# Performance work log

Measured on AMD Instinct MI355X. Metric: run time of the kernel, lower is better.

## Reference

```python
import jax, jax.numpy as jnp
import numpy as np
from jax import lax

N = 256        # graph nodes (== conv5 channels)
C = 128        # diff-pool clusters
E = 4096       # number of edges
EPS = 1e-15    # PyG dense_diff_pool entropy eps


def setup_inputs():
    key = jax.random.key(0)
    ks = jax.random.split(key, 24)
    def rn(k, shape, scale):
        return jax.random.normal(k, shape, dtype=jnp.float32) * scale
    inp = {
        "inputs": jax.random.normal(ks[0], (1, 3, 512, 512), dtype=jnp.float32),
        "edge_index": jax.random.randint(ks[1], (2, E), 0, N, dtype=jnp.int32),
    }
    convs = [(3, 32), (32, 64), (64, 128), (128, 256), (256, 256)]
    for i, (ci, co) in enumerate(convs):
        inp[f"w{i+1}"] = rn(ks[2 + i], (co, ci, 3, 3), 0.05)
        inp[f"b{i+1}"] = jnp.zeros((co,), jnp.float32)
    sages = [(256, 2), (256, 128), (2, 2)]
    for i, (ci, co) in enumerate(sages):
        inp[f"s{i+1}_wl"] = rn(ks[10 + 3 * i], (ci, co), 0.1)
        inp[f"s{i+1}_wr"] = rn(ks[11 + 3 * i], (ci, co), 0.1)
        inp[f"s{i+1}_b"] = jnp.zeros((co,), jnp.float32)
    return inp


def _conv_block(x, w, b):
    # 3x3 SAME conv -> relu -> 2x2 max pool (stride 2), NCHW layout
    x = lax.conv_general_dilated(x, w, (1, 1), 'SAME',
                                 dimension_numbers=('NCHW', 'OIHW', 'NCHW'))
    x = jax.nn.relu(x + b[None, :, None, None])
    return lax.reduce_window(x, -jnp.inf, lax.max,
                             (1, 1, 2, 2), (1, 1, 2, 2), 'VALID')


def _sage(x, src, dst, wl, wr, b, n):
    # PyG SAGEConv(normalize=False): lin_l(mean_{src->dst} x_src) + lin_r(x)
    tot = jax.ops.segment_sum(x[src], dst, num_segments=n)
    cnt = jax.ops.segment_sum(jnp.ones((dst.shape[0],), x.dtype), dst, num_segments=n)
    agg = jnp.where(cnt[:, None] > 0, tot / jnp.maximum(cnt, 1.0)[:, None], 0.0)
    return agg @ wl + b + x @ wr


def reference(inputs, edge_index, w1, b1, w2, b2, w3, b3, w4, b4, w5, b5,
              s1_wl, s1_wr, s1_b, s2_wl, s2_wr, s2_b, s3_wl, s3_wr, s3_b):
    x = inputs
    for w, b in ((w1, b1), (w2, b2), (w3, b3), (w4, b4), (w5, b5)):
        x = _conv_block(x, w, b)
    org = x.reshape(N, N)  # (256 channels, 16*16 spatial) -> node features
    src, dst = edge_index[0], edge_index[1]
    x1 = _sage(org, src, dst, s1_wl, s1_wr, s1_b, N)  # (256, 2)
    s = _sage(org, src, dst, s2_wl, s2_wr, s2_b, N)   # (256, 128)
    # dense adjacency (duplicate edges accumulate, matching scipy coo.todense())
    adj = jnp.zeros((N, N), org.dtype).at[src, dst].add(1.0)
    # dense_diff_pool
    s_soft = jax.nn.softmax(s, axis=-1)
    x_pool = s_soft.T @ x1               # (128, 2)
    adj_pool = s_soft.T @ adj @ s_soft   # (128, 128)
    link_loss = jnp.linalg.norm(adj - s_soft @ s_soft.T) / (N * N)
    ent_loss = (-s_soft * jnp.log(s_soft + EPS)).sum(-1).mean()
    nodes = jnp.tanh(x_pool)             # (128, 2)
    # per-row argmax-equality thresholding (vectorized: rows are independent)
    row_max = adj_pool.max(axis=1, keepdims=True)
    edge_bin = (adj_pool == row_max).astype(org.dtype)  # (128, 128)
    # sage3 over the binarized dense adjacency (equivalent to dense_to_sparse + SAGEConv)
    indeg = edge_bin.sum(axis=0)
    agg = jnp.where(indeg[:, None] > 0,
                    (edge_bin.T @ nodes) / jnp.maximum(indeg, 1.0)[:, None], 0.0)
    out = agg @ s3_wl + s3_b + nodes @ s3_wr  # (128, 2)
    return out.reshape(-1), link_loss, ent_loss, nodes, edge_bin
```

## Files before the change

kernel.cpp:

```cpp
#include <hip/hip_runtime.h>
#include <math.h>

#define NN 256
#define NE 4096
#define NC 128

using short8  = __attribute__((ext_vector_type(8))) short;
using short4v = __attribute__((ext_vector_type(4))) short;
using f32x4   = __attribute__((ext_vector_type(4))) float;

static __device__ __forceinline__ unsigned short f2bf(float x) {
    unsigned u = __float_as_uint(x);
    unsigned r = (u + 0x7FFF + ((u >> 16) & 1)) >> 16;
    return (unsigned short)r;
}

static __device__ __forceinline__ float block_sum_256(float v, float* red4) {
    #pragma unroll
    for (int o = 32; o > 0; o >>= 1) v += __shfl_xor(v, o);
    __syncthreads();
    if ((threadIdx.x & 63) == 0) red4[threadIdx.x >> 6] = v;
    __syncthreads();
    return (red4[0] + red4[1]) + (red4[2] + red4[3]);
}

__global__ void wfrag_zero_all(const float* __restrict__ w1, const float* __restrict__ w2,
                               const float* __restrict__ w3, const float* __restrict__ w4,
                               const float* __restrict__ w5,
                               unsigned short* __restrict__ f1, unsigned short* __restrict__ f2,
                               unsigned short* __restrict__ f3, unsigned short* __restrict__ f4,
                               unsigned short* __restrict__ f5, float* __restrict__ adjz)
{
    int b = blockIdx.x;
    if (b >= 478) {
        adjz[(b - 478) * 256 + threadIdx.x] = 0.f;
        return;
    }
    if (b == 477) {
        int idx = threadIdx.x;
        int lane = idx & 63, rest = idx >> 6;
        int g = rest & 1, slot = rest >> 1;
        int oc = g * 16 + (lane & 15);
        short8 v;
        #pragma unroll
        for (int j = 0; j < 8; ++j) {
            int k = (lane >> 4) * 8 + j;
            float wv = 0.f;
            if (slot == 0) {
                int tap = k >> 2, ch = k & 3;
                if (ch < 3) wv = w1[oc * 27 + ch * 9 + tap];
            } else {
                if (k < 3) wv = w1[oc * 27 + k * 9 + 8];
            }
            v[j] = (short)f2bf(wv);
        }
        *(short8*)&f1[(size_t)idx * 8] = v;
        return;
    }
    const float* w; unsigned short* f; int CIN, NG, NCH, base;
    if (b < 9)        { w = w2; f = f2; CIN = 32;  NG = 4;  NCH = 1; base = 0;   }
    else if (b < 45)  { w = w3; f = f3; CIN = 64;  NG = 8;  NCH = 2; base = 9;   }
    else if (b < 189) { w = w4; f = f4; CIN = 128; NG = 16; NCH = 4; base = 45;  }
    else              { w = w5; f = f5; CIN = 256; NG = 16; NCH = 8; base = 189; }
    int idx = (b - base) * 256 + threadIdx.x;
    int lane = idx & 63, rest = idx >> 6;
    int c = rest % NCH; rest /= NCH;
    int g = rest % NG;  int t = rest / NG;
    if (t >= 9) return;
    int oc = g * 16 + (lane & 15);
    int cin0 = c * 32 + (lane >> 4) * 8;
    short8 v;
    #pragma unroll
    for (int j = 0; j < 8; ++j) {
        v[j] = (short)f2bf(w[((size_t)oc * CIN + cin0 + j) * 9 + t]);
    }
    *(short8*)&f[(size_t)idx * 8] = v;
}

__global__ __launch_bounds__(256) void conv1_adj_kernel(
    const float* __restrict__ in, const unsigned short* __restrict__ wf1,
    const float* __restrict__ bias, unsigned short* __restrict__ out,
    const int* __restrict__ src, const int* __restrict__ dst,
    float* __restrict__ adj, float* __restrict__ adjT)
{
    const int bid = blockIdx.x;
    const int tid = threadIdx.x;
    if (bid >= 2048) {
        int e = (bid - 2048) * 256 + tid;
        int s = src[e], d = dst[e];
        atomicAdd(&adj[s * NN + d], 1.0f);
        atomicAdd(&adjT[d * NN + s], 1.0f);
        return;
    }
    constexpr int Hc = 512;
    const int lane = tid & 63, wid = tid >> 6;
    const int col = lane & 15, kgl = lane >> 4;
    const int X0 = (bid & 31) * 16, Y0 = (bid >> 5) * 8;
    __shared__ __align__(16) unsigned short lds[10][18][4];
    if (tid < 180) {
        int hy = tid / 18, hx = tid - hy * 18;
        int gy = Y0 + hy - 1, gx = X0 + hx - 1;
        float v0 = 0.f, v1 = 0.f, v2 = 0.f;
        if (gy >= 0 && gy < Hc && gx >= 0 && gx < Hc) {
            v0 = in[0 * 262144 + gy * 512 + gx];
            v1 = in[1 * 262144 + gy * 512 + gx];
            v2 = in[2 * 262144 + gy * 512 + gx];
        }
        uint2 uu;
        uu.x = f2bf(v0) | ((unsigned)f2bf(v1) << 16);
        uu.y = f2bf(v2);
        *(uint2*)&lds[hy][hx][0] = uu;
    }
    short8 af[2][2];
    #pragma unroll
    for (int slot = 0; slot < 2; ++slot) {
        #pragma unroll
        for (int g = 0; g < 2; ++g) {
            af[slot][g] = *(const short8*)&wf1[((size_t)((slot * 2 + g) * 64 + lane)) * 8];
        }
    }
    __syncthreads();
    f32x4 acc[2][2];
    #pragma unroll
    for (int g = 0; g < 2; ++g) {
        #pragma unroll
        for (int r = 0; r < 2; ++r) acc[g][r] = {0.f, 0.f, 0.f, 0.f};
    }
    const int t0 = 2 * kgl, t1 = 2 * kgl + 1;
    const int dy0 = t0 / 3, dx0 = t0 % 3, dy1 = t1 / 3, dx1 = t1 % 3;
    #pragma unroll
    for (int r = 0; r < 2; ++r) {
        const int py = wid * 2 + r;
        short4v lo = *(const short4v*)&lds[py + dy0][col + dx0][0];
        short4v hi = *(const short4v*)&lds[py + dy1][col + dx1][0];
        short8 bf0 = __builtin_shufflevector(lo, hi, 0, 1, 2, 3, 4, 5, 6, 7);
        short4v z4 = {0, 0, 0, 0};
        short4v t8 = z4;
        if (kgl == 0) t8 = *(const short4v*)&lds[py + 2][col + 2][0];
        short8 bf1 = __builtin_shufflevector(t8, z4, 0, 1, 2, 3, 4, 5, 6, 7);
        #pragma unroll
        for (int g = 0; g < 2; ++g) {
            acc[g][r] = __builtin_amdgcn_mfma_f32_16x16x32_bf16(af[0][g], bf0, acc[g][r], 0, 0, 0);
            acc[g][r] = __builtin_amdgcn_mfma_f32_16x16x32_bf16(af[1][g], bf1, acc[g][r], 0, 0, 0);
        }
    }
    #pragma unroll
    for (int g = 0; g < 2; ++g) {
        const int oc = g * 16 + kgl * 4;
        const float4 bb = *(const float4*)&bias[oc];
        const float bbv[4] = {bb.x, bb.y, bb.z, bb.w};
        float vv[4];
        #pragma unroll
        for (int q = 0; q < 4; ++q) {
            float v = fmaxf(acc[g][0][q], acc[g][1][q]);
            v = fmaxf(v, __shfl_xor(v, 1));
            vv[q] = fmaxf(v + bbv[q], 0.f);
        }
        if (!(col & 1)) {
            unsigned u0 = f2bf(vv[0]) | ((unsigned)f2bf(vv[1]) << 16);
            unsigned u1 = f2bf(vv[2]) | ((unsigned)f2bf(vv[3]) << 16);
            const int pry = Y0 / 2 + wid;
            const int prx = X0 / 2 + (col >> 1);
            uint2 uu; uu.x = u0; uu.y = u1;
            *(uint2*)&out[((size_t)(pry * 256 + prx)) * 32 + oc] = uu;
        }
    }
}

template<int CIN, int COUT, int Hc, int OCB, int CSPLIT>
__global__ __launch_bounds__(256) void conv_mfma(
    const unsigned short* __restrict__ in, const unsigned short* __restrict__ wfrag,
    const float* __restrict__ bias, void* __restrict__ outv)
{
    constexpr int TR = 8;
    constexpr int NOG = OCB / 16;
    constexpr int NG  = COUT / 16;
    constexpr int NCHT = CIN / 32;
    constexpr int NCH = NCHT / CSPLIT;
    constexpr int RPW = 2;
    constexpr int ITEMS = (TR + 2) * 18 * 4;
    constexpr int NIT = 3;
    const int tid = threadIdx.x;
    const int lane = tid & 63, wid = tid >> 6;
    const int col = lane & 15, kgl = lane >> 4;
    const int X0 = blockIdx.x * 16, Y0 = blockIdx.y * TR;
    const int ob = blockIdx.z / CSPLIT, cs = blockIdx.z % CSPLIT;

    __shared__ __align__(16) unsigned short lds[2][ITEMS * 8];

    int ioff[NIT]; bool ival[NIT]; int loff[NIT];
    #pragma unroll
    for (int it = 0; it < NIT; ++it) {
        int i = tid + it * 256;
        int kg = i & 3, rem = i >> 2;
        int hx = rem % 18, hy = rem / 18;
        int gy = Y0 + hy - 1, gx = X0 + hx - 1;
        ival[it] = (i < ITEMS) && gy >= 0 && gy < Hc && gx >= 0 && gx < Hc;
        ioff[it] = (gy * Hc + gx) * CIN + kg * 8;
        loff[it] = ((hy * 4 + kg) * 18 + hx) * 8;
    }
    short8 sreg[NIT];
    auto sload = [&](int ca) {
        #pragma unroll
        for (int it = 0; it < NIT; ++it) {
            short8 v = {0, 0, 0, 0, 0, 0, 0, 0};
            if (ival[it]) v = *(const short8*)&in[ioff[it] + ca * 32];
            sreg[it] = v;
        }
    };
    auto swrite = [&](int buf) {
        #pragma unroll
        for (int it = 0; it < NIT; ++it) {
            if (tid + it * 256 < ITEMS) *(short8*)&lds[buf][loff[it]] = sreg[it];
        }
    };

    f32x4 acc[NOG][RPW];
    #pragma unroll
    for (int g = 0; g < NOG; ++g) {
        #pragma unroll
        for (int r = 0; r < RPW; ++r) acc[g][r] = {0.f, 0.f, 0.f, 0.f};
    }

    sload(cs * NCH);
    swrite(0);
    __syncthreads();
    for (int cc = 0; cc < NCH; ++cc) {
        const int ca = cs * NCH + cc;
        if (cc + 1 < NCH) sload(ca + 1);
        const unsigned short* L = &lds[cc & 1][0];
        #pragma unroll
        for (int t = 0; t < 9; ++t) {
            const int ky = t / 3, kx = t % 3;
            short8 af[NOG];
            #pragma unroll
            for (int g = 0; g < NOG; ++g) {
                af[g] = *(const short8*)&wfrag[((((size_t)t * NG + ob * NOG + g) * NCHT + ca) * 64 + lane) * 8];
            }
            #pragma unroll
            for (int r = 0; r < RPW; ++r) {
                const int py = wid * RPW + r;
                short8 bf = *(const short8*)&L[(((py + ky) * 4 + kgl) * 18 + col + kx) * 8];
                #pragma unroll
                for (int g = 0; g < NOG; ++g) {
                    acc[g][r] = __builtin_amdgcn_mfma_f32_16x16x32_bf16(af[g], bf, acc[g][r], 0, 0, 0);
                }
            }
        }
        if (cc + 1 < NCH) { swrite((cc + 1) & 1); __syncthreads(); }
    }

    if constexpr (CSPLIT == 1) {
        constexpr int Wp = Hc / 2;
        unsigned short* outp = (unsigned short*)outv;
        #pragma unroll
        for (int g = 0; g < NOG; ++g) {
            const int oc = (ob * NOG + g) * 16 + kgl * 4;
            const float4 bb = *(const float4*)&bias[oc];
            const float bbv[4] = {bb.x, bb.y, bb.z, bb.w};
            float vv[4];
            #pragma unroll
            for (int q = 0; q < 4; ++q) {
                float v = fmaxf(acc[g][0][q], acc[g][1][q]);
                v = fmaxf(v, __shfl_xor(v, 1));
                vv[q] = fmaxf(v + bbv[q], 0.f);
            }
            if (!(col & 1)) {
                unsigned u0 = f2bf(vv[0]) | ((unsigned)f2bf(vv[1]) << 16);
                unsigned u1 = f2bf(vv[2]) | ((unsigned)f2bf(vv[3]) << 16);
                const int pry = Y0 / 2 + wid;
                const int prx = X0 / 2 + (col >> 1);
                uint2 uu; uu.x = u0; uu.y = u1;
                *(uint2*)&outp[((size_t)(pry * Wp + prx)) * COUT + oc] = uu;
            }
        }
    } else {
        float* po = (float*)outv;
        #pragma unroll
        for (int g = 0; g < NOG; ++g) {
            #pragma unroll
            for (int r = 0; r < RPW; ++r) {
                const int gy = Y0 + wid * RPW + r;
                #pragma unroll
                for (int q = 0; q < 4; ++q) {
                    const int oc = (ob * NOG + g) * 16 + kgl * 4 + q;
                    po[((size_t)(cs * COUT + oc) * Hc + gy) * Hc + X0 + col] = acc[g][r][q];
                }
            }
        }
    }
}

template<int COUT, int HP, int CS>
__global__ void finalize_pool(const float* __restrict__ partial, const float* __restrict__ bias,
                              float* __restrict__ out)
{
    int idx = blockIdx.x * 256 + threadIdx.x;
    if (idx >= COUT * HP * HP) return;
    constexpr int H = HP * 2;
    int x = idx & (HP - 1); int rest = idx / HP;
    int y = rest & (HP - 1); int oc = rest / HP;
    float v00 = 0.f, v01 = 0.f, v10 = 0.f, v11 = 0.f;
    #pragma unroll
    for (int cs = 0; cs < CS; ++cs) {
        const float* p = partial + ((size_t)(cs * COUT + oc) * H + 2 * y) * H + 2 * x;
        v00 += p[0]; v01 += p[1]; v10 += p[H]; v11 += p[H + 1];
    }
    float m = fmaxf(fmaxf(v00, v01), fmaxf(v10, v11)) + bias[oc];
    out[idx] = fmaxf(m, 0.f);
}


__global__ __launch_bounds__(256) void node_fused_kernel(
    const float* __restrict__ adjT, const float* __restrict__ org,
    const float* __restrict__ s1wl, const float* __restrict__ s1wr, const float* __restrict__ s1b,
    const float* __restrict__ s2wl, const float* __restrict__ s2wr, const float* __restrict__ s2b,
    float* __restrict__ s_soft, float* __restrict__ s_softT,
    float* __restrict__ x1g, float* __restrict__ entp)
{
    int n = blockIdx.x, t = threadIdx.x;
    __shared__ float rowT[256], orgn[256], aggn[256], red[256], sm[128], red4[4];
    float rT = adjT[n * 256 + t];
    rowT[t] = rT; orgn[t] = org[n * 256 + t];
    __syncthreads();
    float cnt = block_sum_256(rT, red4);
    float a0 = 0.f, a1 = 0.f, a2 = 0.f, a3 = 0.f;
    #pragma unroll 8
    for (int s = 0; s < 256; s += 4) {
        a0 = fmaf(rowT[s + 0], org[(s + 0) * 256 + t], a0);
        a1 = fmaf(rowT[s + 1], org[(s + 1) * 256 + t], a1);
        a2 = fmaf(rowT[s + 2], org[(s + 2) * 256 + t], a2);
        a3 = fmaf(rowT[s + 3], org[(s + 3) * 256 + t], a3);
    }
    float acc = (a0 + a1) + (a2 + a3);
    float aggv = (cnt > 0.f) ? acc / cnt : 0.f;
    aggn[t] = aggv;
    float orgv = orgn[t];
    float x10 = block_sum_256(aggv * s1wl[2 * t] + orgv * s1wr[2 * t], red4) + s1b[0];
    float x11 = block_sum_256(aggv * s1wl[2 * t + 1] + orgv * s1wr[2 * t + 1], red4) + s1b[1];
    if (t == 0) { x1g[n * 2 + 0] = x10; x1g[n * 2 + 1] = x11; }
    int p = t & 127, h = t >> 7;
    float b0 = 0.f, b1 = 0.f, b2 = 0.f, b3 = 0.f;
    #pragma unroll 8
    for (int k = h * 128; k < h * 128 + 128; k += 2) {
        b0 = fmaf(aggn[k],     s2wl[k * NC + p],       b0);
        b1 = fmaf(orgn[k],     s2wr[k * NC + p],       b1);
        b2 = fmaf(aggn[k + 1], s2wl[(k + 1) * NC + p], b2);
        b3 = fmaf(orgn[k + 1], s2wr[(k + 1) * NC + p], b3);
    }
    red[t] = (b0 + b1) + (b2 + b3);
    __syncthreads();
    if (t < 128) sm[p] = red[t] + red[t + 128] + s2b[p];
    __syncthreads();
    if (t < 128) red[t] = sm[t];
    __syncthreads();
    for (int s = 64; s > 0; s >>= 1) { if (t < s) red[t] = fmaxf(red[t], red[t + s]); __syncthreads(); }
    float mx = red[0];
    __syncthreads();
    float e = 0.f;
    if (t < 128) { e = expf(sm[t] - mx); red[t] = e; } else { red[t] = 0.f; }
    __syncthreads();
    for (int s = 64; s > 0; s >>= 1) { if (t < s) red[t] += red[t + s]; __syncthreads(); }
    float denom = red[0];
    float q = e / denom;
    if (t < 128) {
        s_soft[n * NC + t] = q;
        s_softT[t * 256 + n] = q;
    }
    float ev = (t < 128) ? -q * logf(q + 1e-15f) : 0.f;
    float esum = block_sum_256(ev, red4);
    if (t == 0) entp[n] = esum;
}

__global__ __launch_bounds__(256) void row_fused_kernel(
    const float* __restrict__ adj, const float* __restrict__ s_soft,
    const float* __restrict__ s_softT, float* __restrict__ T, float* __restrict__ lpart)
{
    int i = blockIdx.x, j = threadIdx.x;
    __shared__ float si[NC], adjrow[256], tbuf[256], red4[4];
    adjrow[j] = adj[i * 256 + j];
    if (j < NC) si[j] = s_soft[i * NC + j];
    __syncthreads();
    float d0 = 0.f, d1 = 0.f, d2 = 0.f, d3 = 0.f;
    #pragma unroll 8
    for (int k = 0; k < NC; k += 4) {
        d0 = fmaf(si[k + 0], s_softT[(k + 0) * 256 + j], d0);
        d1 = fmaf(si[k + 1], s_softT[(k + 1) * 256 + j], d1);
        d2 = fmaf(si[k + 2], s_softT[(k + 2) * 256 + j], d2);
        d3 = fmaf(si[k + 3], s_softT[(k + 3) * 256 + j], d3);
    }
    float dot = (d0 + d1) + (d2 + d3);
    float dd = adjrow[j] - dot;
    float lsum = block_sum_256(dd * dd, red4);
    if (j == 0) lpart[i] = lsum;
    int p = j & 127, h = j >> 7;
    float a0 = 0.f, a1 = 0.f;
    #pragma unroll 8
    for (int k = h * 128; k < h * 128 + 128; k += 2) {
        a0 = fmaf(adjrow[k],     s_soft[k * NC + p],       a0);
        a1 = fmaf(adjrow[k + 1], s_soft[(k + 1) * NC + p], a1);
    }
    tbuf[j] = a0 + a1;
    __syncthreads();
    if (j < 128) T[i * NC + j] = tbuf[j] + tbuf[j + 128];
}

__global__ __launch_bounds__(256) void cluster_fused_kernel(
    const float* __restrict__ s_softT, const float* __restrict__ T, const float* __restrict__ x1g,
    float* __restrict__ eb_out, float* __restrict__ nodes_out)
{
    int c = blockIdx.x, t = threadIdx.x;
    __shared__ float colc[256], red[256], ap[NC], red4[4];
    colc[t] = s_softT[c * 256 + t];
    __syncthreads();
    int p = t & 127, h = t >> 7;
    float a0 = 0.f, a1 = 0.f;
    #pragma unroll 8
    for (int n = h * 128; n < h * 128 + 128; n += 2) {
        a0 = fmaf(colc[n],     T[n * NC + p],       a0);
        a1 = fmaf(colc[n + 1], T[(n + 1) * NC + p], a1);
    }
    red[t] = a0 + a1;
    __syncthreads();
    if (t < 128) ap[t] = red[t] + red[t + 128];
    __syncthreads();
    if (t < 128) red[t] = ap[t];
    __syncthreads();
    for (int s = 64; s > 0; s >>= 1) { if (t < s) red[t] = fmaxf(red[t], red[t + s]); __syncthreads(); }
    float mx = red[0];
    if (t < 128) eb_out[c * NC + t] = (ap[t] == mx) ? 1.f : 0.f;
    float n0 = tanhf(block_sum_256(colc[t] * x1g[t * 2 + 0], red4));
    float n1 = tanhf(block_sum_256(colc[t] * x1g[t * 2 + 1], red4));
    if (t == 0) { nodes_out[c * 2 + 0] = n0; nodes_out[c * 2 + 1] = n1; }
}

__global__ __launch_bounds__(256) void final_kernel(
    const float* __restrict__ lpart, const float* __restrict__ entp,
    const float* __restrict__ eb, const float* __restrict__ nodes,
    const float* __restrict__ wl, const float* __restrict__ wr, const float* __restrict__ b,
    float* __restrict__ out_main, float* __restrict__ out_link, float* __restrict__ out_ent)
{
    int t = threadIdx.x;
    __shared__ float red4[4];
    float ls = block_sum_256(lpart[t], red4);
    if (t == 0) out_link[0] = sqrtf(ls) / (float)(NN * NN);
    float es = block_sum_256(entp[t], red4);
    if (t == 0) out_ent[0] = es / (float)NN;
    if (t < NC) {
        int j = t;
        float i0 = 0.f, i1 = 0.f, a00 = 0.f, a01 = 0.f, a10 = 0.f, a11 = 0.f;
        #pragma unroll 8
        for (int i2 = 0; i2 < NC; i2 += 2) {
            float e0 = eb[i2 * NC + j];
            float e1 = eb[(i2 + 1) * NC + j];
            i0 += e0; i1 += e1;
            a00 = fmaf(e0, nodes[i2 * 2 + 0], a00);
            a01 = fmaf(e0, nodes[i2 * 2 + 1], a01);
            a10 = fmaf(e1, nodes[(i2 + 1) * 2 + 0], a10);
            a11 = fmaf(e1, nodes[(i2 + 1) * 2 + 1], a11);
        }
        float indeg = i0 + i1;
        float a0 = a00 + a10, a1 = a01 + a11;
        float inv = (indeg > 0.f) ? 1.f / fmaxf(indeg, 1.f) : 0.f;
        float g0 = a0 * inv, g1 = a1 * inv;
        float n0 = nodes[j * 2 + 0], n1 = nodes[j * 2 + 1];
        out_main[j * 2 + 0] = g0 * wl[0] + g1 * wl[2] + b[0] + n0 * wr[0] + n1 * wr[2];
        out_main[j * 2 + 1] = g0 * wl[1] + g1 * wl[3] + b[1] + n0 * wr[1] + n1 * wr[3];
    }
}

extern "C" void kernel_launch(void* const* d_in, const int* in_sizes, int n_in,
                              void* d_out, int out_size, void* d_ws, size_t ws_size,
                              hipStream_t stream)
{
    const float* input = (const float*)d_in[0];
    const int* eidx = (const int*)d_in[1];
    const int* src = eidx;
    const int* dst = eidx + NE;
    const float* w1 = (const float*)d_in[2];  const float* b1 = (const float*)d_in[3];
    const float* w2 = (const float*)d_in[4];  const float* b2 = (const float*)d_in[5];
    const float* w3 = (const float*)d_in[6];  const float* b3 = (const float*)d_in[7];
    const float* w4 = (const float*)d_in[8];  const float* b4 = (const float*)d_in[9];
    const float* w5 = (const float*)d_in[10]; const float* b5 = (const float*)d_in[11];
    const float* s1_wl = (const float*)d_in[12]; const float* s1_wr = (const float*)d_in[13];
    const float* s1_b  = (const float*)d_in[14];
    const float* s2_wl = (const float*)d_in[15]; const float* s2_wr = (const float*)d_in[16];
    const float* s2_b  = (const float*)d_in[17];
    const float* s3_wl = (const float*)d_in[18]; const float* s3_wr = (const float*)d_in[19];
    const float* s3_b  = (const float*)d_in[20];

    float* ws = (float*)d_ws;
    unsigned short* c1 = (unsigned short*)(ws);
    unsigned short* c2 = (unsigned short*)(ws + 1048576);
    unsigned short* c3 = (unsigned short*)(ws);
    unsigned short* c4 = (unsigned short*)(ws + 1048576);
    float* P5  = ws;
    float* ORG = ws + 1179648;
    unsigned short* f1 = (unsigned short*)(ws + 1572864);
    unsigned short* f2 = (unsigned short*)(ws + 1573888);
    unsigned short* f3 = (unsigned short*)(ws + 1583104);
    unsigned short* f4 = (unsigned short*)(ws + 1619968);
    unsigned short* f5 = (unsigned short*)(ws + 1767424);
    float* adj     = ws + 2062336;
    float* adjT    = ws + 2127872;
    float* s_soft  = ws + 2193408;
    float* T       = ws + 2226176;
    float* x1g     = ws + 2258944;
    float* lpart   = ws + 2259456;
    float* entp    = ws + 2259712;
    float* s_softT = ws + 2259968;

    float* fout = (float*)d_out;
    float* out_main  = fout;
    float* out_link  = fout + 256;
    float* out_ent   = fout + 257;
    float* out_nodes = fout + 258;
    float* out_eb    = fout + 514;

    wfrag_zero_all<<<990, 256, 0, stream>>>(w1, w2, w3, w4, w5, f1, f2, f3, f4, f5, adj);
    conv1_adj_kernel<<<2064, 256, 0, stream>>>(input, f1, b1, c1, src, dst, adj, adjT);
    conv_mfma<32,  64, 256, 64, 1><<<dim3(16, 32, 1), 256, 0, stream>>>(c1, f2, b2, c2);
    conv_mfma<64, 128, 128, 64, 1><<<dim3(8, 16, 2),  256, 0, stream>>>(c2, f3, b3, c3);
    conv_mfma<128, 256, 64, 32, 1><<<dim3(4, 8, 8),   256, 0, stream>>>(c3, f4, b4, c4);
    conv_mfma<256, 256, 32, 32, 4><<<dim3(2, 4, 32),  256, 0, stream>>>(c4, f5, b5, P5);
    finalize_pool<256, 16, 4><<<256, 256, 0, stream>>>(P5, b5, ORG);

    node_fused_kernel<<<256, 256, 0, stream>>>(adjT, ORG, s1_wl, s1_wr, s1_b,
                                               s2_wl, s2_wr, s2_b, s_soft, s_softT, x1g, entp);
    row_fused_kernel<<<256, 256, 0, stream>>>(adj, s_soft, s_softT, T, lpart);
    cluster_fused_kernel<<<128, 256, 0, stream>>>(s_softT, T, x1g, out_eb, out_nodes);
    final_kernel<<<1, 256, 0, stream>>>(lpart, entp, out_eb, out_nodes,
                                        s3_wl, s3_wr, s3_b, out_main, out_link, out_ent);
}
```

Measured before the change: 101.2 us.

## Fuse weight prep, adjacency build and conv1 into one kernel; drop conv5 split-K

Merges the weight-fragment packing, adjacency zeroing and atomic scatter, and conv1 into a single launch. Adjacency rows are now built per node in shared-memory counters, so no global zeroing or global atomics are needed. conv1 converts its own weights in-register. conv5 drops its channel split plus the separate finalize_pool pass and writes the pooled fp32 output directly, while the OCB tiles shrink to raise block counts. This saves launches and partial-sum traffic, but each adjacency block rescans all edges and conv5 loses split-K parallelism.

Result: slower. 111.7 us (+10.4%).

```diff
diff --git a/kernel.cpp b/kernel.cpp
--- a/kernel.cpp
+++ b/kernel.cpp
@@ -24,72 +24,55 @@
     return (red4[0] + red4[1]) + (red4[2] + red4[3]);
 }
 
-__global__ void wfrag_zero_all(const float* __restrict__ w1, const float* __restrict__ w2,
-                               const float* __restrict__ w3, const float* __restrict__ w4,
-                               const float* __restrict__ w5,
-                               unsigned short* __restrict__ f1, unsigned short* __restrict__ f2,
-                               unsigned short* __restrict__ f3, unsigned short* __restrict__ f4,
-                               unsigned short* __restrict__ f5, float* __restrict__ adjz)
-{
-    int b = blockIdx.x;
-    if (b >= 478) {
-        adjz[(b - 478) * 256 + threadIdx.x] = 0.f;
-        return;
-    }
-    if (b == 477) {
-        int idx = threadIdx.x;
-        int lane = idx & 63, rest = idx >> 6;
-        int g = rest & 1, slot = rest >> 1;
-        int oc = g * 16 + (lane & 15);
-        short8 v;
-        #pragma unroll
-        for (int j = 0; j < 8; ++j) {
-            int k = (lane >> 4) * 8 + j;
-            float wv = 0.f;
-            if (slot == 0) {
-                int tap = k >> 2, ch = k & 3;
-                if (ch < 3) wv = w1[oc * 27 + ch * 9 + tap];
-            } else {
-                if (k < 3) wv = w1[oc * 27 + k * 9 + 8];
-            }
-            v[j] = (short)f2bf(wv);
-        }
-        *(short8*)&f1[(size_t)idx * 8] = v;
-        return;
-    }
-    const float* w; unsigned short* f; int CIN, NG, NCH, base;
-    if (b < 9)        { w = w2; f = f2; CIN = 32;  NG = 4;  NCH = 1; base = 0;   }
-    else if (b < 45)  { w = w3; f = f3; CIN = 64;  NG = 8;  NCH = 2; base = 9;   }
-    else if (b < 189) { w = w4; f = f4; CIN = 128; NG = 16; NCH = 4; base = 45;  }
-    else              { w = w5; f = f5; CIN = 256; NG = 16; NCH = 8; base = 189; }
-    int idx = (b - base) * 256 + threadIdx.x;
-    int lane = idx & 63, rest = idx >> 6;
-    int c = rest % NCH; rest /= NCH;
-    int g = rest % NG;  int t = rest / NG;
-    if (t >= 9) return;
-    int oc = g * 16 + (lane & 15);
-    int cin0 = c * 32 + (lane >> 4) * 8;
-    short8 v;
-    #pragma unroll
-    for (int j = 0; j < 8; ++j) {
-        v[j] = (short)f2bf(w[((size_t)oc * CIN + cin0 + j) * 9 + t]);
-    }
-    *(short8*)&f[(size_t)idx * 8] = v;
-}
-
-__global__ __launch_bounds__(256) void conv1_adj_kernel(
-    const float* __restrict__ in, const unsigned short* __restrict__ wf1,
-    const float* __restrict__ bias, unsigned short* __restrict__ out,
+__global__ __launch_bounds__(256) void mega1_kernel(
+    const float* __restrict__ in, const float* __restrict__ w1, const float* __restrict__ bias1,
+    unsigned short* __restrict__ c1out,
+    const float* __restrict__ w2, const float* __restrict__ w3, const float* __restrict__ w4,
+    const float* __restrict__ w5,
+    unsigned short* __restrict__ f2, unsigned short* __restrict__ f3,
+    unsigned short* __restrict__ f4, unsigned short* __restrict__ f5,
     const int* __restrict__ src, const int* __restrict__ dst,
     float* __restrict__ adj, float* __restrict__ adjT)
 {
     const int bid = blockIdx.x;
     const int tid = threadIdx.x;
+    if (bid >= 2525) {
+        __shared__ int cntA[256], cntT[256];
+        const int n = bid - 2525;
+        cntA[tid] = 0; cntT[tid] = 0;
+        __syncthreads();
+        #pragma unroll
+        for (int i = 0; i < 16; ++i) {
+            int e = tid + i * 256;
+            int s = src[e], d = dst[e];
+            if (s == n) atomicAdd(&cntA[d], 1);
+            if (d == n) atomicAdd(&cntT[s], 1);
+        }
+        __syncthreads();
+        adj[n * NN + tid]  = (float)cntA[tid];
+        adjT[n * NN + tid] = (float)cntT[tid];
+        return;
+    }
     if (bid >= 2048) {
-        int e = (bid - 2048) * 256 + tid;
-        int s = src[e], d = dst[e];
-        atomicAdd(&adj[s * NN + d], 1.0f);
-        atomicAdd(&adjT[d * NN + s], 1.0f);
+        int b = bid - 2048;
+        const float* w; unsigned short* f; int CIN, NG, NCH, base;
+        if (b < 9)        { w = w2; f = f2; CIN = 32;  NG = 4;  NCH = 1; base = 0;   }
+        else if (b < 45)  { w = w3; f = f3; CIN = 64;  NG = 8;  NCH = 2; base = 9;   }
+        else if (b < 189) { w = w4; f = f4; CIN = 128; NG = 16; NCH = 4; base = 45;  }
+        else              { w = w5; f = f5; CIN = 256; NG = 16; NCH = 8; base = 189; }
+        int idx = (b - base) * 256 + tid;
+        int lane = idx & 63, rest = idx >> 6;
+        int c = rest % NCH; rest /= NCH;
+        int g = rest % NG;  int t = rest / NG;
+        if (t >= 9) return;
+        int oc = g * 16 + (lane & 15);
+        int cin0 = c * 32 + (lane >> 4) * 8;
+        short8 v;
+        #pragma unroll
+        for (int j = 0; j < 8; ++j) {
+            v[j] = (short)f2bf(w[((size_t)oc * CIN + cin0 + j) * 9 + t]);
+        }
+        *(short8*)&f[(size_t)idx * 8] = v;
         return;
     }
     constexpr int Hc = 512;
@@ -116,7 +99,21 @@
     for (int slot = 0; slot < 2; ++slot) {
         #pragma unroll
         for (int g = 0; g < 2; ++g) {
-            af[slot][g] = *(const short8*)&wf1[((size_t)((slot * 2 + g) * 64 + lane)) * 8];
+            int oc = g * 16 + (lane & 15);
+            short8 v;
+            #pragma unroll
+            for (int j = 0; j < 8; ++j) {
+                int k = (lane >> 4) * 8 + j;
+                float wv = 0.f;
+                if (slot == 0) {
+                    int tap = k >> 2, ch = k & 3;
+                    if (ch < 3) wv = w1[oc * 27 + ch * 9 + tap];
+                } else {
+                    if (k < 3) wv = w1[oc * 27 + k * 9 + 8];
+                }
+                v[j] = (short)f2bf(wv);
+            }
+            af[slot][g] = v;
         }
     }
     __syncthreads();
@@ -147,7 +144,7 @@
     #pragma unroll
     for (int g = 0; g < 2; ++g) {
         const int oc = g * 16 + kgl * 4;
-        const float4 bb = *(const float4*)&bias[oc];
+        const float4 bb = *(const float4*)&bias1[oc];
         const float bbv[4] = {bb.x, bb.y, bb.z, bb.w};
         float vv[4];
         #pragma unroll
@@ -162,12 +159,12 @@
             const int pry = Y0 / 2 + wid;
             const int prx = X0 / 2 + (col >> 1);
             uint2 uu; uu.x = u0; uu.y = u1;
-            *(uint2*)&out[((size_t)(pry * 256 + prx)) * 32 + oc] = uu;
-        }
-    }
-}
-
-template<int CIN, int COUT, int Hc, int OCB, int CSPLIT>
+            *(uint2*)&c1out[((size_t)(pry * 256 + prx)) * 32 + oc] = uu;
+        }
+    }
+}
+
+template<int CIN, int COUT, int Hc, int OCB, int OMODE>
 __global__ __launch_bounds__(256) void conv_mfma(
     const unsigned short* __restrict__ in, const unsigned short* __restrict__ wfrag,
     const float* __restrict__ bias, void* __restrict__ outv)
@@ -175,8 +172,7 @@
     constexpr int TR = 8;
     constexpr int NOG = OCB / 16;
     constexpr int NG  = COUT / 16;
-    constexpr int NCHT = CIN / 32;
-    constexpr int NCH = NCHT / CSPLIT;
+    constexpr int NCH = CIN / 32;
     constexpr int RPW = 2;
     constexpr int ITEMS = (TR + 2) * 18 * 4;
     constexpr int NIT = 3;
@@ -184,7 +180,7 @@
     const int lane = tid & 63, wid = tid >> 6;
     const int col = lane & 15, kgl = lane >> 4;
     const int X0 = blockIdx.x * 16, Y0 = blockIdx.y * TR;
-    const int ob = blockIdx.z / CSPLIT, cs = blockIdx.z % CSPLIT;
+    const int ob = blockIdx.z;
 
     __shared__ __align__(16) unsigned short lds[2][ITEMS * 8];
 
@@ -222,12 +218,11 @@
         for (int r = 0; r < RPW; ++r) acc[g][r] = {0.f, 0.f, 0.f, 0.f};
     }
 
-    sload(cs * NCH);
+    sload(0);
     swrite(0);
     __syncthreads();
     for (int cc = 0; cc < NCH; ++cc) {
-        const int ca = cs * NCH + cc;
-        if (cc + 1 < NCH) sload(ca + 1);
+        if (cc + 1 < NCH) sload(cc + 1);
         const unsigned short* L = &lds[cc & 1][0];
         #pragma unroll
         for (int t = 0; t < 9; ++t) {
@@ -235,7 +230,7 @@
             short8 af[NOG];
             #pragma unroll
             for (int g = 0; g < NOG; ++g) {
-                af[g] = *(const short8*)&wfrag[((((size_t)t * NG + ob * NOG + g) * NCHT + ca) * 64 + lane) * 8];
+                af[g] = *(const short8*)&wfrag[((((size_t)t * NG + ob * NOG + g) * NCH + cc) * 64 + lane) * 8];
             }
             #pragma unroll
             for (int r = 0; r < RPW; ++r) {
@@ -250,64 +245,36 @@
         if (cc + 1 < NCH) { swrite((cc + 1) & 1); __syncthreads(); }
     }
 
-    if constexpr (CSPLIT == 1) {
-        constexpr int Wp = Hc / 2;
-        unsigned short* outp = (unsigned short*)outv;
-        #pragma unroll
-        for (int g = 0; g < NOG; ++g) {
-            const int oc = (ob * NOG + g) * 16 + kgl * 4;
-            const float4 bb = *(const float4*)&bias[oc];
-            const float bbv[4] = {bb.x, bb.y, bb.z, bb.w};
-            float vv[4];
-            #pragma unroll
-            for (int q = 0; q < 4; ++q) {
-                float v = fmaxf(acc[g][0][q], acc[g][1][q]);
-                v = fmaxf(v, __shfl_xor(v, 1));
-                vv[q] = fmaxf(v + bbv[q], 0.f);
-            }
-            if (!(col & 1)) {
+    constexpr int Wp = Hc / 2;
+    #pragma unroll
+    for (int g = 0; g < NOG; ++g) {
+        const int oc = (ob * NOG + g) * 16 + kgl * 4;
+        const float4 bb = *(const float4*)&bias[oc];
+        const float bbv[4] = {bb.x, bb.y, bb.z, bb.w};
+        float vv[4];
+        #pragma unroll
+        for (int q = 0; q < 4; ++q) {
+            float v = fmaxf(acc[g][0][q], acc[g][1][q]);
+            v = fmaxf(v, __shfl_xor(v, 1));
+            vv[q] = fmaxf(v + bbv[q], 0.f);
+        }
+        if (!(col & 1)) {
+            const int pry = Y0 / 2 + wid;
+            const int prx = X0 / 2 + (col >> 1);
+            if constexpr (OMODE == 0) {
                 unsigned u0 = f2bf(vv[0]) | ((unsigned)f2bf(vv[1]) << 16);
                 unsigned u1 = f2bf(vv[2]) | ((unsigned)f2bf(vv[3]) << 16);
-                const int pry = Y0 / 2 + wid;
-                const int prx = X0 / 2 + (col >> 1);
                 uint2 uu; uu.x = u0; uu.y = u1;
-                *(uint2*)&outp[((size_t)(pry * Wp + prx)) * COUT + oc] = uu;
-            }
-        }
-    } else {
-        float* po = (float*)outv;
-        #pragma unroll
-        for (int g = 0; g < NOG; ++g) {
-            #pragma unroll
-            for (int r = 0; r < RPW; ++r) {
-                const int gy = Y0 + wid * RPW + r;
+                *(uint2*)&((unsigned short*)outv)[((size_t)(pry * Wp + prx)) * COUT + oc] = uu;
+            } else {
+                float* po = (float*)outv;
                 #pragma unroll
                 for (int q = 0; q < 4; ++q) {
-                    const int oc = (ob * NOG + g) * 16 + kgl * 4 + q;
-                    po[((size_t)(cs * COUT + oc) * Hc + gy) * Hc + X0 + col] = acc[g][r][q];
+                    po[(size_t)(oc + q) * (Wp * Wp) + pry * Wp + prx] = vv[q];
                 }
             }
         }
     }
-}
-
-template<int COUT, int HP, int CS>
-__global__ void finalize_pool(const float* __restrict__ partial, const float* __restrict__ bias,
-                              float* __restrict__ out)
-{
-    int idx = blockIdx.x * 256 + threadIdx.x;
-    if (idx >= COUT * HP * HP) return;
-    constexpr int H = HP * 2;
-    int x = idx & (HP - 1); int rest = idx / HP;
-    int y = rest & (HP - 1); int oc = rest / HP;
-    float v00 = 0.f, v01 = 0.f, v10 = 0.f, v11 = 0.f;
-    #pragma unroll
-    for (int cs = 0; cs < CS; ++cs) {
-        const float* p = partial + ((size_t)(cs * COUT + oc) * H + 2 * y) * H + 2 * x;
-        v00 += p[0]; v01 += p[1]; v10 += p[H]; v11 += p[H + 1];
-    }
-    float m = fmaxf(fmaxf(v00, v01), fmaxf(v10, v11)) + bias[oc];
-    out[idx] = fmaxf(m, 0.f);
 }
 
 
@@ -494,9 +461,7 @@
     unsigned short* c2 = (unsigned short*)(ws + 1048576);
     unsigned short* c3 = (unsigned short*)(ws);
     unsigned short* c4 = (unsigned short*)(ws + 1048576);
-    float* P5  = ws;
     float* ORG = ws + 1179648;
-    unsigned short* f1 = (unsigned short*)(ws + 1572864);
     unsigned short* f2 = (unsigned short*)(ws + 1573888);
     unsigned short* f3 = (unsigned short*)(ws + 1583104);
     unsigned short* f4 = (unsigned short*)(ws + 1619968);
@@ -517,13 +482,12 @@
     float* out_nodes = fout + 258;
     float* out_eb    = fout + 514;
 
-    wfrag_zero_all<<<990, 256, 0, stream>>>(w1, w2, w3, w4, w5, f1, f2, f3, f4, f5, adj);
-    conv1_adj_kernel<<<2064, 256, 0, stream>>>(input, f1, b1, c1, src, dst, adj, adjT);
-    conv_mfma<32,  64, 256, 64, 1><<<dim3(16, 32, 1), 256, 0, stream>>>(c1, f2, b2, c2);
-    conv_mfma<64, 128, 128, 64, 1><<<dim3(8, 16, 2),  256, 0, stream>>>(c2, f3, b3, c3);
-    conv_mfma<128, 256, 64, 32, 1><<<dim3(4, 8, 8),   256, 0, stream>>>(c3, f4, b4, c4);
-    conv_mfma<256, 256, 32, 32, 4><<<dim3(2, 4, 32),  256, 0, stream>>>(c4, f5, b5, P5);
-    finalize_pool<256, 16, 4><<<256, 256, 0, stream>>>(P5, b5, ORG);
+    mega1_kernel<<<2781, 256, 0, stream>>>(input, w1, b1, c1, w2, w3, w4, w5,
+                                           f2, f3, f4, f5, src, dst, adj, adjT);
+    conv_mfma<32,  64, 256, 32, 0><<<dim3(16, 32, 2), 256, 0, stream>>>(c1, f2, b2, c2);
+    conv_mfma<64, 128, 128, 32, 0><<<dim3(8, 16, 4),  256, 0, stream>>>(c2, f3, b3, c3);
+    conv_mfma<128, 256, 64, 16, 0><<<dim3(4, 8, 16),  256, 0, stream>>>(c3, f4, b4, c4);
+    conv_mfma<256, 256, 32, 16, 2><<<dim3(2, 4, 16),  256, 0, stream>>>(c4, f5, b5, ORG);
 
     node_fused_kernel<<<256, 256, 0, stream>>>(adjT, ORG, s1_wl, s1_wr, s1_b,
                                                s2_wl, s2_wr, s2_b, s_soft, s_softT, x1g, entp);
```

## Merge weight prep, adjacency build and conv1 into one launch

Applied to the files above, without the earlier changes.

Folds the weight-fragment conversion kernel into the conv1 launch as extra blocks, and has each conv1 block compute its w1 fragments directly from fp32 weights instead of reading a prepared buffer. The adjacency matrices are now built per row with LDS counters scanning all edges, instead of being zeroed and filled with global atomics, which removes the zeroing pass and the dependency between launches. This saves one kernel launch and a global atomic phase, at the cost of redundant w1 conversion in every conv1 block and 256 blocks each scanning all 4096 edges.

After: 105.0 us, median of 2. 3.8% more time.

```diff
diff --git a/kernel.cpp b/kernel.cpp
--- a/kernel.cpp
+++ b/kernel.cpp
@@ -24,72 +24,55 @@
     return (red4[0] + red4[1]) + (red4[2] + red4[3]);
 }
 
-__global__ void wfrag_zero_all(const float* __restrict__ w1, const float* __restrict__ w2,
-                               const float* __restrict__ w3, const float* __restrict__ w4,
-                               const float* __restrict__ w5,
-                               unsigned short* __restrict__ f1, unsigned short* __restrict__ f2,
-                               unsigned short* __restrict__ f3, unsigned short* __restrict__ f4,
-                               unsigned short* __restrict__ f5, float* __restrict__ adjz)
-{
-    int b = blockIdx.x;
-    if (b >= 478) {
-        adjz[(b - 478) * 256 + threadIdx.x] = 0.f;
-        return;
-    }
-    if (b == 477) {
-        int idx = threadIdx.x;
-        int lane = idx & 63, rest = idx >> 6;
-        int g = rest & 1, slot = rest >> 1;
-        int oc = g * 16 + (lane & 15);
-        short8 v;
-        #pragma unroll
-        for (int j = 0; j < 8; ++j) {
-            int k = (lane >> 4) * 8 + j;
-            float wv = 0.f;
-            if (slot == 0) {
-                int tap = k >> 2, ch = k & 3;
-                if (ch < 3) wv = w1[oc * 27 + ch * 9 + tap];
-            } else {
-                if (k < 3) wv = w1[oc * 27 + k * 9 + 8];
-            }
-            v[j] = (short)f2bf(wv);
-        }
-        *(short8*)&f1[(size_t)idx * 8] = v;
-        return;
-    }
-    const float* w; unsigned short* f; int CIN, NG, NCH, base;
-    if (b < 9)        { w = w2; f = f2; CIN = 32;  NG = 4;  NCH = 1; base = 0;   }
-    else if (b < 45)  { w = w3; f = f3; CIN = 64;  NG = 8;  NCH = 2; base = 9;   }
-    else if (b < 189) { w = w4; f = f4; CIN = 128; NG = 16; NCH = 4; base = 45;  }
-    else              { w = w5; f = f5; CIN = 256; NG = 16; NCH = 8; base = 189; }
-    int idx = (b - base) * 256 + threadIdx.x;
-    int lane = idx & 63, rest = idx >> 6;
-    int c = rest % NCH; rest /= NCH;
-    int g = rest % NG;  int t = rest / NG;
-    if (t >= 9) return;
-    int oc = g * 16 + (lane & 15);
-    int cin0 = c * 32 + (lane >> 4) * 8;
-    short8 v;
-    #pragma unroll
-    for (int j = 0; j < 8; ++j) {
-        v[j] = (short)f2bf(w[((size_t)oc * CIN + cin0 + j) * 9 + t]);
-    }
-    *(short8*)&f[(size_t)idx * 8] = v;
-}
-
-__global__ __launch_bounds__(256) void conv1_adj_kernel(
-    const float* __restrict__ in, const unsigned short* __restrict__ wf1,
-    const float* __restrict__ bias, unsigned short* __restrict__ out,
+__global__ __launch_bounds__(256) void mega1_kernel(
+    const float* __restrict__ in, const float* __restrict__ w1, const float* __restrict__ bias1,
+    unsigned short* __restrict__ c1out,
+    const float* __restrict__ w2, const float* __restrict__ w3, const float* __restrict__ w4,
+    const float* __restrict__ w5,
+    unsigned short* __restrict__ f2, unsigned short* __restrict__ f3,
+    unsigned short* __restrict__ f4, unsigned short* __restrict__ f5,
     const int* __restrict__ src, const int* __restrict__ dst,
     float* __restrict__ adj, float* __restrict__ adjT)
 {
     const int bid = blockIdx.x;
     const int tid = threadIdx.x;
+    if (bid >= 2525) {
+        __shared__ int cntA[256], cntT[256];
+        const int n = bid - 2525;
+        cntA[tid] = 0; cntT[tid] = 0;
+        __syncthreads();
+        #pragma unroll
+        for (int i = 0; i < 16; ++i) {
+            int e = tid + i * 256;
+            int s = src[e], d = dst[e];
+            if (s == n) atomicAdd(&cntA[d], 1);
+            if (d == n) atomicAdd(&cntT[s], 1);
+        }
+        __syncthreads();
+        adj[n * NN + tid]  = (float)cntA[tid];
+        adjT[n * NN + tid] = (float)cntT[tid];
+        return;
+    }
     if (bid >= 2048) {
-        int e = (bid - 2048) * 256 + tid;
-        int s = src[e], d = dst[e];
-        atomicAdd(&adj[s * NN + d], 1.0f);
-        atomicAdd(&adjT[d * NN + s], 1.0f);
+        int b = bid - 2048;
+        const float* w; unsigned short* f; int CIN, NG, NCH, base;
+        if (b < 9)        { w = w2; f = f2; CIN = 32;  NG = 4;  NCH = 1; base = 0;   }
+        else if (b < 45)  { w = w3; f = f3; CIN = 64;  NG = 8;  NCH = 2; base = 9;   }
+        else if (b < 189) { w = w4; f = f4; CIN = 128; NG = 16; NCH = 4; base = 45;  }
+        else              { w = w5; f = f5; CIN = 256; NG = 16; NCH = 8; base = 189; }
+        int idx = (b - base) * 256 + tid;
+        int lane = idx & 63, rest = idx >> 6;
+        int c = rest % NCH; rest /= NCH;
+        int g = rest % NG;  int t = rest / NG;
+        if (t >= 9) return;
+        int oc = g * 16 + (lane & 15);
+        int cin0 = c * 32 + (lane >> 4) * 8;
+        short8 v;
+        #pragma unroll
+        for (int j = 0; j < 8; ++j) {
+            v[j] = (short)f2bf(w[((size_t)oc * CIN + cin0 + j) * 9 + t]);
+        }
+        *(short8*)&f[(size_t)idx * 8] = v;
         return;
     }
     constexpr int Hc = 512;
@@ -116,7 +99,21 @@
     for (int slot = 0; slot < 2; ++slot) {
         #pragma unroll
         for (int g = 0; g < 2; ++g) {
-            af[slot][g] = *(const short8*)&wf1[((size_t)((slot * 2 + g) * 64 + lane)) * 8];
+            int oc = g * 16 + (lane & 15);
+            short8 v;
+            #pragma unroll
+            for (int j = 0; j < 8; ++j) {
+                int k = (lane >> 4) * 8 + j;
+                float wv = 0.f;
+                if (slot == 0) {
+                    int tap = k >> 2, ch = k & 3;
+                    if (ch < 3) wv = w1[oc * 27 + ch * 9 + tap];
+                } else {
+                    if (k < 3) wv = w1[oc * 27 + k * 9 + 8];
+                }
+                v[j] = (short)f2bf(wv);
+            }
+            af[slot][g] = v;
         }
     }
     __syncthreads();
@@ -147,7 +144,7 @@
     #pragma unroll
     for (int g = 0; g < 2; ++g) {
         const int oc = g * 16 + kgl * 4;
-        const float4 bb = *(const float4*)&bias[oc];
+        const float4 bb = *(const float4*)&bias1[oc];
         const float bbv[4] = {bb.x, bb.y, bb.z, bb.w};
         float vv[4];
         #pragma unroll
@@ -162,7 +159,7 @@
             const int pry = Y0 / 2 + wid;
             const int prx = X0 / 2 + (col >> 1);
             uint2 uu; uu.x = u0; uu.y = u1;
-            *(uint2*)&out[((size_t)(pry * 256 + prx)) * 32 + oc] = uu;
+            *(uint2*)&c1out[((size_t)(pry * 256 + prx)) * 32 + oc] = uu;
         }
     }
 }
@@ -496,7 +493,6 @@
     unsigned short* c4 = (unsigned short*)(ws + 1048576);
     float* P5  = ws;
     float* ORG = ws + 1179648;
-    unsigned short* f1 = (unsigned short*)(ws + 1572864);
     unsigned short* f2 = (unsigned short*)(ws + 1573888);
     unsigned short* f3 = (unsigned short*)(ws + 1583104);
     unsigned short* f4 = (unsigned short*)(ws + 1619968);
@@ -517,8 +513,8 @@
     float* out_nodes = fout + 258;
     float* out_eb    = fout + 514;
 
-    wfrag_zero_all<<<990, 256, 0, stream>>>(w1, w2, w3, w4, w5, f1, f2, f3, f4, f5, adj);
-    conv1_adj_kernel<<<2064, 256, 0, stream>>>(input, f1, b1, c1, src, dst, adj, adjT);
+    mega1_kernel<<<2781, 256, 0, stream>>>(input, w1, b1, c1, w2, w3, w4, w5,
+                                           f2, f3, f4, f5, src, dst, adj, adjT);
     conv_mfma<32,  64, 256, 64, 1><<<dim3(16, 32, 1), 256, 0, stream>>>(c1, f2, b2, c2);
     conv_mfma<64, 128, 128, 64, 1><<<dim3(8, 16, 2),  256, 0, stream>>>(c2, f3, b3, c3);
     conv_mfma<128, 256, 64, 32, 1><<<dim3(4, 8, 8),   256, 0, stream>>>(c3, f4, b4, c4);
```

## Build adjacency via per-row shared counts, enlarge conv1 tiles, retune conv5 split

Applied to the files above, without the earlier changes.

The dense adjacency and its transpose are now built in the prep kernel. Each of 256 blocks scans all edges and counts in shared memory, which replaces the zero-fill plus global float atomics that ran inside conv1. Conv1 now processes 16x16 output tiles per block (4 rows per wave) instead of 16x8, halving the block count and reusing the weight fragments across more pixels. Conv5 switches to a 16-channel output block with a channel split of 2, and the pool finalization is adjusted to match. Each adjacency block re-reads every edge, which adds redundant reads of the edge list in exchange for avoiding contended global atomics.

Result: slower. 107.7 us (+6.4%).

```diff
diff --git a/kernel.cpp b/kernel.cpp
--- a/kernel.cpp
+++ b/kernel.cpp
@@ -24,21 +24,36 @@
     return (red4[0] + red4[1]) + (red4[2] + red4[3]);
 }
 
-__global__ void wfrag_zero_all(const float* __restrict__ w1, const float* __restrict__ w2,
-                               const float* __restrict__ w3, const float* __restrict__ w4,
-                               const float* __restrict__ w5,
-                               unsigned short* __restrict__ f1, unsigned short* __restrict__ f2,
-                               unsigned short* __restrict__ f3, unsigned short* __restrict__ f4,
-                               unsigned short* __restrict__ f5, float* __restrict__ adjz)
+__global__ void prep_kernel(const float* __restrict__ w1, const float* __restrict__ w2,
+                            const float* __restrict__ w3, const float* __restrict__ w4,
+                            const float* __restrict__ w5,
+                            unsigned short* __restrict__ f1, unsigned short* __restrict__ f2,
+                            unsigned short* __restrict__ f3, unsigned short* __restrict__ f4,
+                            unsigned short* __restrict__ f5,
+                            const int* __restrict__ src, const int* __restrict__ dst,
+                            float* __restrict__ adj, float* __restrict__ adjT)
 {
     int b = blockIdx.x;
+    int tid = threadIdx.x;
     if (b >= 478) {
-        adjz[(b - 478) * 256 + threadIdx.x] = 0.f;
+        __shared__ int cntA[256], cntT[256];
+        const int n = b - 478;
+        cntA[tid] = 0; cntT[tid] = 0;
+        __syncthreads();
+        #pragma unroll
+        for (int i = 0; i < 16; ++i) {
+            int e = tid + i * 256;
+            int s = src[e], d = dst[e];
+            if (s == n) atomicAdd(&cntA[d], 1);
+            if (d == n) atomicAdd(&cntT[s], 1);
+        }
+        __syncthreads();
+        adj[n * NN + tid]  = (float)cntA[tid];
+        adjT[n * NN + tid] = (float)cntT[tid];
         return;
     }
     if (b == 477) {
-        int idx = threadIdx.x;
-        int lane = idx & 63, rest = idx >> 6;
+        int lane = tid & 63, rest = tid >> 6;
         int g = rest & 1, slot = rest >> 1;
         int oc = g * 16 + (lane & 15);
         short8 v;
@@ -54,7 +69,7 @@
             }
             v[j] = (short)f2bf(wv);
         }
-        *(short8*)&f1[(size_t)idx * 8] = v;
+        *(short8*)&f1[(size_t)tid * 8] = v;
         return;
     }
     const float* w; unsigned short* f; int CIN, NG, NCH, base;
@@ -62,7 +77,7 @@
     else if (b < 45)  { w = w3; f = f3; CIN = 64;  NG = 8;  NCH = 2; base = 9;   }
     else if (b < 189) { w = w4; f = f4; CIN = 128; NG = 16; NCH = 4; base = 45;  }
     else              { w = w5; f = f5; CIN = 256; NG = 16; NCH = 8; base = 189; }
-    int idx = (b - base) * 256 + threadIdx.x;
+    int idx = (b - base) * 256 + tid;
     int lane = idx & 63, rest = idx >> 6;
     int c = rest % NCH; rest /= NCH;
     int g = rest % NG;  int t = rest / NG;
@@ -77,28 +92,18 @@
     *(short8*)&f[(size_t)idx * 8] = v;
 }
 
-__global__ __launch_bounds__(256) void conv1_adj_kernel(
+__global__ __launch_bounds__(256) void conv1_kernel(
     const float* __restrict__ in, const unsigned short* __restrict__ wf1,
-    const float* __restrict__ bias, unsigned short* __restrict__ out,
-    const int* __restrict__ src, const int* __restrict__ dst,
-    float* __restrict__ adj, float* __restrict__ adjT)
-{
-    const int bid = blockIdx.x;
+    const float* __restrict__ bias, unsigned short* __restrict__ out)
+{
+    constexpr int Hc = 512;
     const int tid = threadIdx.x;
-    if (bid >= 2048) {
-        int e = (bid - 2048) * 256 + tid;
-        int s = src[e], d = dst[e];
-        atomicAdd(&adj[s * NN + d], 1.0f);
-        atomicAdd(&adjT[d * NN + s], 1.0f);
-        return;
-    }
-    constexpr int Hc = 512;
     const int lane = tid & 63, wid = tid >> 6;
     const int col = lane & 15, kgl = lane >> 4;
-    const int X0 = (bid & 31) * 16, Y0 = (bid >> 5) * 8;
-    __shared__ __align__(16) unsigned short lds[10][18][4];
-    if (tid < 180) {
-        int hy = tid / 18, hx = tid - hy * 18;
+    const int X0 = blockIdx.x * 16, Y0 = blockIdx.y * 16;
+    __shared__ __align__(16) unsigned short lds[18][18][4];
+    for (int i = tid; i < 324; i += 256) {
+        int hy = i / 18, hx = i - hy * 18;
         int gy = Y0 + hy - 1, gx = X0 + hx - 1;
         float v0 = 0.f, v1 = 0.f, v2 = 0.f;
         if (gy >= 0 && gy < Hc && gx >= 0 && gx < Hc) {
@@ -120,17 +125,17 @@
         }
     }
     __syncthreads();
-    f32x4 acc[2][2];
+    f32x4 acc[2][4];
     #pragma unroll
     for (int g = 0; g < 2; ++g) {
         #pragma unroll
-        for (int r = 0; r < 2; ++r) acc[g][r] = {0.f, 0.f, 0.f, 0.f};
+        for (int r = 0; r < 4; ++r) acc[g][r] = {0.f, 0.f, 0.f, 0.f};
     }
     const int t0 = 2 * kgl, t1 = 2 * kgl + 1;
     const int dy0 = t0 / 3, dx0 = t0 % 3, dy1 = t1 / 3, dx1 = t1 % 3;
     #pragma unroll
-    for (int r = 0; r < 2; ++r) {
-        const int py = wid * 2 + r;
+    for (int r = 0; r < 4; ++r) {
+        const int py = wid * 4 + r;
         short4v lo = *(const short4v*)&lds[py + dy0][col + dx0][0];
         short4v hi = *(const short4v*)&lds[py + dy1][col + dx1][0];
         short8 bf0 = __builtin_shufflevector(lo, hi, 0, 1, 2, 3, 4, 5, 6, 7);
@@ -149,20 +154,23 @@
         const int oc = g * 16 + kgl * 4;
         const float4 bb = *(const float4*)&bias[oc];
         const float bbv[4] = {bb.x, bb.y, bb.z, bb.w};
-        float vv[4];
-        #pragma unroll
-        for (int q = 0; q < 4; ++q) {
-            float v = fmaxf(acc[g][0][q], acc[g][1][q]);
-            v = fmaxf(v, __shfl_xor(v, 1));
-            vv[q] = fmaxf(v + bbv[q], 0.f);
-        }
-        if (!(col & 1)) {
-            unsigned u0 = f2bf(vv[0]) | ((unsigned)f2bf(vv[1]) << 16);
-            unsigned u1 = f2bf(vv[2]) | ((unsigned)f2bf(vv[3]) << 16);
-            const int pry = Y0 / 2 + wid;
-            const int prx = X0 / 2 + (col >> 1);
-            uint2 uu; uu.x = u0; uu.y = u1;
-            *(uint2*)&out[((size_t)(pry * 256 + prx)) * 32 + oc] = uu;
+        #pragma unroll
+        for (int pr = 0; pr < 2; ++pr) {
+            float vv[4];
+            #pragma unroll
+            for (int q = 0; q < 4; ++q) {
+                float v = fmaxf(acc[g][2 * pr][q], acc[g][2 * pr + 1][q]);
+                v = fmaxf(v, __shfl_xor(v, 1));
+                vv[q] = fmaxf(v + bbv[q], 0.f);
+            }
+            if (!(col & 1)) {
+                unsigned u0 = f2bf(vv[0]) | ((unsigned)f2bf(vv[1]) << 16);
+                unsigned u1 = f2bf(vv[2]) | ((unsigned)f2bf(vv[3]) << 16);
+                const int pry = Y0 / 2 + wid * 2 + pr;
+                const int prx = X0 / 2 + (col >> 1);
+                uint2 uu; uu.x = u0; uu.y = u1;
+                *(uint2*)&out[((size_t)(pry * 256 + prx)) * 32 + oc] = uu;
+            }
         }
     }
 }
@@ -517,13 +525,14 @@
     float* out_nodes = fout + 258;
     float* out_eb    = fout + 514;
 
-    wfrag_zero_all<<<990, 256, 0, stream>>>(w1, w2, w3, w4, w5, f1, f2, f3, f4, f5, adj);
-    conv1_adj_kernel<<<2064, 256, 0, stream>>>(input, f1, b1, c1, src, dst, adj, adjT);
+    prep_kernel<<<734, 256, 0, stream>>>(w1, w2, w3, w4, w5, f1, f2, f3, f4, f5,
+                                         src, dst, adj, adjT);
+    conv1_kernel<<<dim3(32, 32), 256, 0, stream>>>(input, f1, b1, c1);
     conv_mfma<32,  64, 256, 64, 1><<<dim3(16, 32, 1), 256, 0, stream>>>(c1, f2, b2, c2);
     conv_mfma<64, 128, 128, 64, 1><<<dim3(8, 16, 2),  256, 0, stream>>>(c2, f3, b3, c3);
     conv_mfma<128, 256, 64, 32, 1><<<dim3(4, 8, 8),   256, 0, stream>>>(c3, f4, b4, c4);
-    conv_mfma<256, 256, 32, 32, 4><<<dim3(2, 4, 32),  256, 0, stream>>>(c4, f5, b5, P5);
-    finalize_pool<256, 16, 4><<<256, 256, 0, stream>>>(P5, b5, ORG);
+    conv_mfma<256, 256, 32, 16, 2><<<dim3(2, 4, 32),  256, 0, stream>>>(c4, f5, b5, P5);
+    finalize_pool<256, 16, 2><<<256, 256, 0, stream>>>(P5, b5, ORG);
 
     node_fused_kernel<<<256, 256, 0, stream>>>(adjT, ORG, s1_wl, s1_wr, s1_b,
                                                s2_wl, s2_wr, s2_b, s_soft, s_softT, x1g, entp);
```
